# Kernel optimization log

Measured on AMD Instinct MI355X. Metric: run time of the kernel, lower is better.

The kernel has to match this reference:

```python
import jax, jax.numpy as jnp
import numpy as np

B, T, V, E, U = 64, 128, 20000, 512, 1024


def _gru_dir(x_tbe, W, Uw, bi, bh):
    """Keras GRU (reset_after=True, gate order z,r,h). x_tbe: [T,B,E]."""
    # Precompute all input projections in one big GEMM: [T,B,3U]
    xg = jnp.einsum('tbe,eg->tbg', x_tbe, W) + bi

    def step(h, xg_t):
        hg = h @ Uw + bh                       # [B,3U]
        xz, xr, xh = jnp.split(xg_t, 3, axis=-1)
        hz, hr, hh = jnp.split(hg, 3, axis=-1)
        z = jax.nn.sigmoid(xz + hz)            # update gate
        r = jax.nn.sigmoid(xr + hr)            # reset gate
        hcand = jnp.tanh(xh + r * hh)          # reset_after=True form
        h_new = z * h + (1.0 - z) * hcand
        return h_new, h_new

    h0 = jnp.zeros((x_tbe.shape[1], Uw.shape[0]), x_tbe.dtype)
    hT, outs = jax.lax.scan(step, h0, xg)      # outs: [T,B,U]
    return outs, hT


def setup_inputs() -> dict:
    key = jax.random.key(0)
    ks = jax.random.split(key, 8)
    s_in = 1.0 / np.sqrt(E)
    s_rec = 1.0 / np.sqrt(U)
    return {
        'tokens': jax.random.randint(ks[0], (B, T), 0, V),
        'emb': jax.random.normal(ks[1], (V, E), jnp.float32) * 0.05,
        'Wf': jax.random.normal(ks[2], (E, 3 * U), jnp.float32) * s_in,
        'Uf': jax.random.normal(ks[3], (U, 3 * U), jnp.float32) * s_rec,
        'bif': jnp.zeros((3 * U,), jnp.float32),
        'bhf': jnp.zeros((3 * U,), jnp.float32),
        'Wb': jax.random.normal(ks[4], (E, 3 * U), jnp.float32) * s_in,
        'Ub': jax.random.normal(ks[5], (U, 3 * U), jnp.float32) * s_rec,
        'bib': jnp.zeros((3 * U,), jnp.float32),
        'bhb': jnp.zeros((3 * U,), jnp.float32),
    }


def reference(tokens, emb, Wf, Uf, bif, bhf, Wb, Ub, bib, bhb):
    tokens = tokens[:, ::-1]                    # tf.reverse(inputs, [-1])
    x = emb[tokens]                             # embedding lookup -> [B,T,E]
    x_t = jnp.swapaxes(x, 0, 1)                 # [T,B,E]
    out_f, h_f = _gru_dir(x_t, Wf, Uf, bif, bhf)
    out_b, h_b = _gru_dir(x_t[::-1], Wb, Ub, bib, bhb)
    out_b = out_b[::-1]                         # re-align backward outputs
    outputs = jnp.swapaxes(out_f + out_b, 0, 1)  # merge_mode='sum' -> [B,T,U]
    hidden = jnp.concatenate([h_f, h_b], axis=1)  # [B,2U]
    return outputs, hidden
```

## Files before the change

kernel.cpp:

```cpp
#include <hip/hip_runtime.h>
#include <hip/hip_bf16.h>

typedef float f32;
typedef __hip_bfloat16 bf16;
typedef unsigned int u32;
typedef unsigned short u16;

#define T_LEN 128
#define B_SZ  64
#define E_DIM 512
#define U_DIM 1024
#define G3    3072
#define BTU   (B_SZ * T_LEN * U_DIM)

typedef __attribute__((ext_vector_type(8))) __bf16 bf16x8;
typedef __attribute__((ext_vector_type(8))) u16  us8;
typedef __attribute__((ext_vector_type(4))) u16  us4;
typedef __attribute__((ext_vector_type(4))) f32  f32x4;

union F8 { us8 u; bf16x8 b; };

#define WS_USW 0u
#define WS_HQ  25165824u
#define WS_XG  26214400u

#define STEP_LDS 98304
#define XG_LDS   66048

__device__ __forceinline__ u32 f32_to_bf16_rne(f32 x) {
  u32 b = __float_as_uint(x);
  return (b + 0x7fffu + ((b >> 16) & 1u)) >> 16;
}

__global__ __launch_bounds__(256) void transpose_split(
    const f32* __restrict__ Uf, const f32* __restrict__ Ub, u16* __restrict__ USW)
{
  __shared__ f32 tile[32][33];
  const int d = blockIdx.z;
  const f32* Uw = d ? Ub : Uf;
  const int c0 = blockIdx.x * 32;
  const int k0 = blockIdx.y * 32;
  const int tx = threadIdx.x & 31;
  const int ty = threadIdx.x >> 5;
#pragma unroll
  for (int i = 0; i < 4; i++) {
    int kl = ty + i * 8;
    tile[kl][tx] = Uw[(size_t)(k0 + kl) * G3 + c0 + tx];
  }
  __syncthreads();
#pragma unroll
  for (int i = 0; i < 4; i++) {
    int cl = ty + i * 8;
    int c  = c0 + cl;
    f32 val = tile[tx][cl];
    int g = c >> 10, u = c & 1023;
    int blk = d * 128 + (u >> 3);
    int r   = g * 8 + (u & 7);
    u32 hib = f32_to_bf16_rne(val);
    f32 rem = val - __uint_as_float(hib << 16);
    u32 lob = f32_to_bf16_rne(rem);
    int k = k0 + tx;
    int slot = (k >> 3) ^ (r & 7);
    size_t base = ((size_t)blk * 2) * (24 * 1024);
    size_t off  = (size_t)r * 1024 + slot * 8 + (k & 7);
    USW[base + off] = (u16)hib;
    USW[base + (size_t)24 * 1024 + off] = (u16)lob;
  }
}

__global__ __launch_bounds__(256) void xg_gemm_mfma(
    const int* __restrict__ tokens, const f32* __restrict__ emb,
    const f32* __restrict__ Wf, const f32* __restrict__ bif,
    const f32* __restrict__ Wb, const f32* __restrict__ bib,
    bf16* __restrict__ XG)
{
  extern __shared__ u16 XL[];
  u16* Ash = XL;
  u16* Bsh = XL + 16384;
  int* tok_s = (int*)(XL + 32768);

  const int tid = threadIdx.x;
  const int n0 = blockIdx.x * 128;
  const int by = blockIdx.y;
  const int dir = by >> 6;
  const int s0 = (by & 63) * 2;
  const f32* W  = dir ? Wb : Wf;
  const f32* bi = dir ? bib : bif;

  if (tid < 128) {
    int srow = s0 + (tid >> 6);
    int b = tid & 63;
    int t_orig = dir ? srow : (T_LEN - 1 - srow);
    tok_s[tid] = tokens[b * T_LEN + t_orig];
  }
  __syncthreads();

  const int wv = tid >> 6;
  const int lane = tid & 63;
  const int arow = tid >> 1;
  const int akoff = (tid & 1) * 32;
  const int bcol = tid & 127;
  const int bkoff = (tid >> 7) * 32;

  f32x4 acc[2][8];
#pragma unroll
  for (int mi = 0; mi < 2; mi++)
#pragma unroll
    for (int ni = 0; ni < 8; ni++) acc[mi][ni] = (f32x4){0.f, 0.f, 0.f, 0.f};

  const f32* asrc0 = emb + (size_t)tok_s[arow] * E_DIM + akoff;

  for (int kk = 0; kk < 8; kk++) {
    __syncthreads();
    {
      const f32* src = asrc0 + kk * 64;
#pragma unroll
      for (int g = 0; g < 4; g++) {
        float4 v0 = *(const float4*)(src + g * 8);
        float4 v1 = *(const float4*)(src + g * 8 + 4);
        f32 vv[8] = {v0.x,v0.y,v0.z,v0.w,v1.x,v1.y,v1.z,v1.w};
        us8 h8, l8;
#pragma unroll
        for (int e = 0; e < 8; e++) {
          u32 bb = __float_as_uint(vv[e]);
          h8[e] = (u16)(bb >> 16);
          f32 rem = vv[e] - __uint_as_float(bb & 0xffff0000u);
          l8[e] = (u16)f32_to_bf16_rne(rem);
        }
        int sl = (((akoff >> 3) + g) ^ (arow & 7)) * 8;
        *(us8*)&Ash[(size_t)arow * 64 + sl] = h8;
        *(us8*)&Ash[(size_t)(128 + arow) * 64 + sl] = l8;
      }
    }
    {
      const f32* src = W + (size_t)(kk * 64 + bkoff) * G3 + n0 + bcol;
#pragma unroll
      for (int g = 0; g < 4; g++) {
        us8 h8, l8;
#pragma unroll
        for (int e = 0; e < 8; e++) {
          f32 v = src[(size_t)(g * 8 + e) * G3];
          u32 bb = __float_as_uint(v);
          h8[e] = (u16)(bb >> 16);
          f32 rem = v - __uint_as_float(bb & 0xffff0000u);
          l8[e] = (u16)f32_to_bf16_rne(rem);
        }
        int sl = (((bkoff >> 3) + g) ^ (bcol & 7)) * 8;
        *(us8*)&Bsh[(size_t)bcol * 64 + sl] = h8;
        *(us8*)&Bsh[(size_t)(128 + bcol) * 64 + sl] = l8;
      }
    }
    __syncthreads();
#pragma unroll
    for (int ks = 0; ks < 2; ks++) {
      F8 ah[2], al[2];
#pragma unroll
      for (int mi = 0; mi < 2; mi++) {
        int row = wv * 32 + mi * 16 + (lane & 15);
        int sl = ((ks * 4 + (lane >> 4)) ^ (row & 7)) * 8;
        ah[mi].u = *(const us8*)&Ash[(size_t)row * 64 + sl];
        al[mi].u = *(const us8*)&Ash[(size_t)(128 + row) * 64 + sl];
      }
#pragma unroll
      for (int ni = 0; ni < 8; ni++) {
        int col = ni * 16 + (lane & 15);
        int sl = ((ks * 4 + (lane >> 4)) ^ (col & 7)) * 8;
        F8 bh, bl;
        bh.u = *(const us8*)&Bsh[(size_t)col * 64 + sl];
        bl.u = *(const us8*)&Bsh[(size_t)(128 + col) * 64 + sl];
#pragma unroll
        for (int mi = 0; mi < 2; mi++) {
          acc[mi][ni] = __builtin_amdgcn_mfma_f32_16x16x32_bf16(ah[mi].b, bh.b, acc[mi][ni], 0, 0, 0);
          acc[mi][ni] = __builtin_amdgcn_mfma_f32_16x16x32_bf16(ah[mi].b, bl.b, acc[mi][ni], 0, 0, 0);
          acc[mi][ni] = __builtin_amdgcn_mfma_f32_16x16x32_bf16(al[mi].b, bh.b, acc[mi][ni], 0, 0, 0);
        }
      }
    }
  }
#pragma unroll
  for (int ni = 0; ni < 8; ni++) {
    int ncol = n0 + ni * 16 + (lane & 15);
    f32 bv = bi[ncol];
#pragma unroll
    for (int mi = 0; mi < 2; mi++) {
#pragma unroll
      for (int j = 0; j < 4; j++) {
        int row = wv * 32 + mi * 16 + (lane >> 4) * 4 + j;
        int srow = s0 + (row >> 6);
        int b = row & 63;
        XG[((size_t)(dir * T_LEN + srow) * B_SZ + b) * G3 + ncol] =
            __float2bfloat16(acc[mi][ni][j] + bv);
      }
    }
  }
}

__global__ __launch_bounds__(512) void gru_step5(
    const u16* __restrict__ USW,
    u32* __restrict__ Hq,
    const u16* __restrict__ XG,
    const f32* __restrict__ bhf, const f32* __restrict__ bhb,
    f32* __restrict__ out, int s)
{
  extern __shared__ u16 Us[];
  const int blk = blockIdx.x;
  const int dir = blk >> 7;
  const int su  = (blk & 127) * 8;
  const int tid = threadIdx.x;
  const int lane = tid & 63;
  const int w  = tid >> 6;
  const int nw = w & 3, kw = w >> 2;

  {
    const us8* src = (const us8*)(USW + (size_t)blk * (2 * 24 * 1024));
    us8* dst = (us8*)Us;
    for (int i = tid; i < 6144; i += 512) dst[i] = src[i];
  }

  const u32* Hin  = Hq + (size_t)((s & 1) * 2 + dir) * (U_DIM * B_SZ);
  u32*       Hout = Hq + (size_t)(((s + 1) & 1) * 2 + dir) * (U_DIM * B_SZ);

  const int bb = nw * 16 + (lane & 15);
  const int ko = (lane >> 4) * 8;
  const int r0 = lane & 15;
  const int r1t = 16 + (lane & 15);
  const int r1 = r1t > 23 ? 23 : r1t;

  const int rb_h0 = (0 * 24 + r0) * 2048;
  const int rb_l0 = (1 * 24 + r0) * 2048;
  const int rb_h1 = (0 * 24 + r1) * 2048;
  const int rb_l1 = (1 * 24 + r1) * 2048;
  const int sw0 = r0 & 7, sw1 = r1 & 7;

  __syncthreads();

  f32x4 acc0 = {0.f, 0.f, 0.f, 0.f};
  f32x4 acc1 = {0.f, 0.f, 0.f, 0.f};

  if (s) {
    for (int ks = 0; ks < 16; ks++) {
      const int kb = kw * 512 + ks * 32;
      const int slot = (kb >> 3) + (lane >> 4);
      F8 ah0, al0, ah1, al1;
      ah0.u = *(const us8*)((const char*)Us + rb_h0 + ((slot ^ sw0) << 4));
      al0.u = *(const us8*)((const char*)Us + rb_l0 + ((slot ^ sw0) << 4));
      ah1.u = *(const us8*)((const char*)Us + rb_h1 + ((slot ^ sw1) << 4));
      al1.u = *(const us8*)((const char*)Us + rb_l1 + ((slot ^ sw1) << 4));

      const int kbase = kb + ko;
      u32 wd[8];
#pragma unroll
      for (int e = 0; e < 8; e++) wd[e] = Hin[(size_t)(kbase + e) * B_SZ + bb];
      F8 bh_hi, bh_lo;
#pragma unroll
      for (int e = 0; e < 8; e++) {
        bh_hi.u[e] = (u16)(wd[e] & 0xffffu);
        bh_lo.u[e] = (u16)(wd[e] >> 16);
      }
      acc0 = __builtin_amdgcn_mfma_f32_16x16x32_bf16(ah0.b, bh_hi.b, acc0, 0, 0, 0);
      acc0 = __builtin_amdgcn_mfma_f32_16x16x32_bf16(ah0.b, bh_lo.b, acc0, 0, 0, 0);
      acc0 = __builtin_amdgcn_mfma_f32_16x16x32_bf16(al0.b, bh_hi.b, acc0, 0, 0, 0);
      acc1 = __builtin_amdgcn_mfma_f32_16x16x32_bf16(ah1.b, bh_hi.b, acc1, 0, 0, 0);
      acc1 = __builtin_amdgcn_mfma_f32_16x16x32_bf16(ah1.b, bh_lo.b, acc1, 0, 0, 0);
      acc1 = __builtin_amdgcn_mfma_f32_16x16x32_bf16(al1.b, bh_hi.b, acc1, 0, 0, 0);
    }
  }

  __syncthreads();
  f32* red = (f32*)Us;
  if (kw == 1) {
    f32* p = red + (size_t)(nw * 64 + lane) * 8;
    *(f32x4*)p = acc0;
    *(f32x4*)(p + 4) = acc1;
  }
  __syncthreads();
  if (kw == 0) {
    const f32* p = red + (size_t)(nw * 64 + lane) * 8;
    f32x4 o0 = *(const f32x4*)p;
    f32x4 o1 = *(const f32x4*)(p + 4);
#pragma unroll
    for (int i = 0; i < 4; i++) { acc0[i] += o0[i]; acc1[i] += o1[i]; }

    f32 racc[4];
#pragma unroll
    for (int j = 0; j < 4; j++) racc[j] = __shfl_xor(acc0[j], 32);

    if (lane < 32) {
      const int ul0 = (lane >> 4) * 4;
      const int u0 = su + ul0;
      const u16* xgp = XG + ((size_t)(dir * T_LEN + s) * B_SZ + bb) * G3;
      us4 gz = *(const us4*)(xgp + u0);
      us4 gr = *(const us4*)(xgp + 1024 + u0);
      us4 gh = *(const us4*)(xgp + 2048 + u0);
      const f32* bh = dir ? bhb : bhf;
      f32x4 hnv;
#pragma unroll
      for (int j = 0; j < 4; j++) {
        const int u = u0 + j;
        f32 hz = acc0[j] + bh[u];
        f32 hr = racc[j] + bh[1024 + u];
        f32 hh = acc1[j] + bh[2048 + u];
        f32 xz = __uint_as_float((u32)gz[j] << 16);
        f32 xr = __uint_as_float((u32)gr[j] << 16);
        f32 xh = __uint_as_float((u32)gh[j] << 16);

        u32 hw = s ? Hin[(size_t)u * B_SZ + bb] : 0u;
        f32 hold = __uint_as_float(hw << 16) + __uint_as_float(hw & 0xffff0000u);

        f32 z  = 1.f / (1.f + expf(-(xz + hz)));
        f32 r  = 1.f / (1.f + expf(-(xr + hr)));
        f32 hc = tanhf(xh + r * hh);
        f32 hnew = z * hold + (1.f - z) * hc;

        u32 hib = f32_to_bf16_rne(hnew);
        f32 rem = hnew - __uint_as_float(hib << 16);
        u32 lob = f32_to_bf16_rne(rem);
        Hout[(size_t)u * B_SZ + bb] = hib | (lob << 16);
        hnv[j] = hnew;
      }

      const int t = dir ? (T_LEN - 1 - s) : s;
      f32* op = out + ((size_t)bb * T_LEN + t) * U_DIM + u0;
      if (s < 64) {
        *(f32x4*)op = hnv;
      } else {
        f32x4 prev = *(const f32x4*)op;
#pragma unroll
        for (int j = 0; j < 4; j++) prev[j] += hnv[j];
        *(f32x4*)op = prev;
      }
      if (s == T_LEN - 1)
        *(f32x4*)(out + (size_t)BTU + (size_t)bb * 2048 + dir * 1024 + u0) = hnv;
    }
  }
}

extern "C" void kernel_launch(void* const* d_in, const int* in_sizes, int n_in,
                              void* d_out, int out_size, void* d_ws, size_t ws_size,
                              hipStream_t stream) {
  (void)in_sizes; (void)n_in; (void)out_size; (void)ws_size;
  const int* tokens = (const int*)d_in[0];
  const f32* emb = (const f32*)d_in[1];
  const f32* Wf  = (const f32*)d_in[2];
  const f32* Uf  = (const f32*)d_in[3];
  const f32* bif = (const f32*)d_in[4];
  const f32* bhf = (const f32*)d_in[5];
  const f32* Wb  = (const f32*)d_in[6];
  const f32* Ub  = (const f32*)d_in[7];
  const f32* bib = (const f32*)d_in[8];
  const f32* bhb = (const f32*)d_in[9];

  char* ws = (char*)d_ws;
  u16*  USW = (u16*)(ws + WS_USW);
  u32*  Hq  = (u32*)(ws + WS_HQ);
  bf16* XG  = (bf16*)(ws + WS_XG);
  f32*  out = (f32*)d_out;

  transpose_split<<<dim3(96, 32, 2), 256, 0, stream>>>(Uf, Ub, USW);

  hipFuncSetAttribute((const void*)xg_gemm_mfma,
                      hipFuncAttributeMaxDynamicSharedMemorySize, XG_LDS);
  xg_gemm_mfma<<<dim3(24, 128), 256, XG_LDS, stream>>>(tokens, emb, Wf, bif, Wb, bib, XG);

  hipFuncSetAttribute((const void*)gru_step5,
                      hipFuncAttributeMaxDynamicSharedMemorySize, STEP_LDS);
  for (int s = 0; s < T_LEN; s++)
    gru_step5<<<256, 512, STEP_LDS, stream>>>(USW, Hq, (const u16*)XG, bhf, bhb, out, s);
}
```

Measured before the change: 1.892 ms.

## Pre-split W and embeddings into bf16 hi/lo; store hidden state batch-major split planes

Adds pre-pass kernels that split W (transposed) and gathered embeddings into bf16 hi/lo planes, staged in the output buffer as scratch. The input-projection GEMM then loads them with vectorized 16-byte reads instead of converting per tile and doing strided column loads of W. The recurrent step kernel now keeps the hidden state as separate hi/lo u16 planes laid out batch-major, so the B operand is two vector loads instead of eight scalar strided u32 loads. This adds extra kernel launches and scratch traffic in exchange for cheaper inner-loop loads.

```diff
diff --git a/kernel.cpp b/kernel.cpp
--- a/kernel.cpp
+++ b/kernel.cpp
@@ -24,8 +24,9 @@
 #define WS_HQ  25165824u
 #define WS_XG  26214400u
 
+
 #define STEP_LDS 98304
-#define XG_LDS   66048
+#define XG_LDS   65536
 
 __device__ __forceinline__ u32 f32_to_bf16_rne(f32 x) {
   u32 b = __float_as_uint(x);
@@ -68,32 +69,74 @@
   }
 }
 
-__global__ __launch_bounds__(256) void xg_gemm_mfma(
-    const int* __restrict__ tokens, const f32* __restrict__ emb,
-    const f32* __restrict__ Wf, const f32* __restrict__ bif,
-    const f32* __restrict__ Wb, const f32* __restrict__ bib,
+__global__ __launch_bounds__(256) void split_w(
+    const f32* __restrict__ Wf, const f32* __restrict__ Wb, u16* __restrict__ WT)
+{
+  __shared__ f32 tile[32][33];
+  const int d = blockIdx.z;
+  const f32* W = d ? Wb : Wf;
+  const int c0 = blockIdx.x * 32;
+  const int k0 = blockIdx.y * 32;
+  const int tx = threadIdx.x & 31;
+  const int ty = threadIdx.x >> 5;
+#pragma unroll
+  for (int i = 0; i < 4; i++) {
+    int kl = ty + i * 8;
+    tile[kl][tx] = W[(size_t)(k0 + kl) * G3 + c0 + tx];
+  }
+  __syncthreads();
+#pragma unroll
+  for (int i = 0; i < 4; i++) {
+    int cl = ty + i * 8;
+    f32 val = tile[tx][cl];
+    u32 bb = __float_as_uint(val);
+    u16 hi = (u16)(bb >> 16);
+    f32 rem = val - __uint_as_float(bb & 0xffff0000u);
+    u16 lo = (u16)f32_to_bf16_rne(rem);
+    size_t ch = (((size_t)(d * 2 + 0) * G3) + c0 + cl) * 512 + k0 + tx;
+    size_t cl_ = (((size_t)(d * 2 + 1) * G3) + c0 + cl) * 512 + k0 + tx;
+    WT[ch] = hi;
+    WT[cl_] = lo;
+  }
+}
+
+__global__ __launch_bounds__(128) void split_emb(
+    const int* __restrict__ tokens, const f32* __restrict__ emb, u16* __restrict__ XE)
+{
+  const int row = blockIdx.x;
+  const int b = row >> 7, t = row & 127;
+  const int tok = tokens[(size_t)b * T_LEN + t];
+  const int k = threadIdx.x * 4;
+  float4 v = *(const float4*)(emb + (size_t)tok * E_DIM + k);
+  f32 vv[4] = {v.x, v.y, v.z, v.w};
+  us4 h4, l4;
+#pragma unroll
+  for (int e = 0; e < 4; e++) {
+    u32 bb = __float_as_uint(vv[e]);
+    h4[e] = (u16)(bb >> 16);
+    f32 rem = vv[e] - __uint_as_float(bb & 0xffff0000u);
+    l4[e] = (u16)f32_to_bf16_rne(rem);
+  }
+  *(us4*)(XE + ((size_t)(0 * 64 + b) * 128 + t) * 512 + k) = h4;
+  *(us4*)(XE + ((size_t)(1 * 64 + b) * 128 + t) * 512 + k) = l4;
+}
+
+__global__ __launch_bounds__(256) void xg_gemm_mfma2(
+    const u16* __restrict__ XE,
+    const u16* __restrict__ WT,
+    const f32* __restrict__ bif, const f32* __restrict__ bib,
     bf16* __restrict__ XG)
 {
   extern __shared__ u16 XL[];
   u16* Ash = XL;
   u16* Bsh = XL + 16384;
-  int* tok_s = (int*)(XL + 32768);
 
   const int tid = threadIdx.x;
   const int n0 = blockIdx.x * 128;
   const int by = blockIdx.y;
   const int dir = by >> 6;
   const int s0 = (by & 63) * 2;
-  const f32* W  = dir ? Wb : Wf;
   const f32* bi = dir ? bib : bif;
-
-  if (tid < 128) {
-    int srow = s0 + (tid >> 6);
-    int b = tid & 63;
-    int t_orig = dir ? srow : (T_LEN - 1 - srow);
-    tok_s[tid] = tokens[b * T_LEN + t_orig];
-  }
-  __syncthreads();
 
   const int wv = tid >> 6;
   const int lane = tid & 63;
@@ -102,53 +145,37 @@
   const int bcol = tid & 127;
   const int bkoff = (tid >> 7) * 32;
 
+  const int srow = s0 + (arow >> 6);
+  const int ab = arow & 63;
+  const int at = dir ? srow : (T_LEN - 1 - srow);
+  const u16* asrc_h = XE + ((size_t)(0 * 64 + ab) * 128 + at) * 512 + akoff;
+  const u16* asrc_l = XE + ((size_t)(1 * 64 + ab) * 128 + at) * 512 + akoff;
+  const u16* bsrc_h = WT + ((size_t)(dir * 2 + 0) * G3 + n0 + bcol) * 512 + bkoff;
+  const u16* bsrc_l = WT + ((size_t)(dir * 2 + 1) * G3 + n0 + bcol) * 512 + bkoff;
+
   f32x4 acc[2][8];
 #pragma unroll
   for (int mi = 0; mi < 2; mi++)
 #pragma unroll
     for (int ni = 0; ni < 8; ni++) acc[mi][ni] = (f32x4){0.f, 0.f, 0.f, 0.f};
-
-  const f32* asrc0 = emb + (size_t)tok_s[arow] * E_DIM + akoff;
 
   for (int kk = 0; kk < 8; kk++) {
     __syncthreads();
-    {
-      const f32* src = asrc0 + kk * 64;
-#pragma unroll
-      for (int g = 0; g < 4; g++) {
-        float4 v0 = *(const float4*)(src + g * 8);
-        float4 v1 = *(const float4*)(src + g * 8 + 4);
-        f32 vv[8] = {v0.x,v0.y,v0.z,v0.w,v1.x,v1.y,v1.z,v1.w};
-        us8 h8, l8;
-#pragma unroll
-        for (int e = 0; e < 8; e++) {
-          u32 bb = __float_as_uint(vv[e]);
-          h8[e] = (u16)(bb >> 16);
-          f32 rem = vv[e] - __uint_as_float(bb & 0xffff0000u);
-          l8[e] = (u16)f32_to_bf16_rne(rem);
-        }
-        int sl = (((akoff >> 3) + g) ^ (arow & 7)) * 8;
-        *(us8*)&Ash[(size_t)arow * 64 + sl] = h8;
-        *(us8*)&Ash[(size_t)(128 + arow) * 64 + sl] = l8;
-      }
-    }
-    {
-      const f32* src = W + (size_t)(kk * 64 + bkoff) * G3 + n0 + bcol;
-#pragma unroll
-      for (int g = 0; g < 4; g++) {
-        us8 h8, l8;
-#pragma unroll
-        for (int e = 0; e < 8; e++) {
-          f32 v = src[(size_t)(g * 8 + e) * G3];
-          u32 bb = __float_as_uint(v);
-          h8[e] = (u16)(bb >> 16);
-          f32 rem = v - __uint_as_float(bb & 0xffff0000u);
-          l8[e] = (u16)f32_to_bf16_rne(rem);
-        }
-        int sl = (((bkoff >> 3) + g) ^ (bcol & 7)) * 8;
-        *(us8*)&Bsh[(size_t)bcol * 64 + sl] = h8;
-        *(us8*)&Bsh[(size_t)(128 + bcol) * 64 + sl] = l8;
-      }
+#pragma unroll
+    for (int g = 0; g < 4; g++) {
+      us8 h8 = *(const us8*)(asrc_h + kk * 64 + g * 8);
+      us8 l8 = *(const us8*)(asrc_l + kk * 64 + g * 8);
+      int sl = (((akoff >> 3) + g) ^ (arow & 7)) * 8;
+      *(us8*)&Ash[(size_t)arow * 64 + sl] = h8;
+      *(us8*)&Ash[(size_t)(128 + arow) * 64 + sl] = l8;
+    }
+#pragma unroll
+    for (int g = 0; g < 4; g++) {
+      us8 h8 = *(const us8*)(bsrc_h + kk * 64 + g * 8);
+      us8 l8 = *(const us8*)(bsrc_l + kk * 64 + g * 8);
+      int sl = (((bkoff >> 3) + g) ^ (bcol & 7)) * 8;
+      *(us8*)&Bsh[(size_t)bcol * 64 + sl] = h8;
+      *(us8*)&Bsh[(size_t)(128 + bcol) * 64 + sl] = l8;
     }
     __syncthreads();
 #pragma unroll
@@ -186,18 +213,18 @@
 #pragma unroll
       for (int j = 0; j < 4; j++) {
         int row = wv * 32 + mi * 16 + (lane >> 4) * 4 + j;
-        int srow = s0 + (row >> 6);
+        int sr = s0 + (row >> 6);
         int b = row & 63;
-        XG[((size_t)(dir * T_LEN + srow) * B_SZ + b) * G3 + ncol] =
+        XG[((size_t)(dir * T_LEN + sr) * B_SZ + b) * G3 + ncol] =
             __float2bfloat16(acc[mi][ni][j] + bv);
       }
     }
   }
 }
 
-__global__ __launch_bounds__(512) void gru_step5(
+__global__ __launch_bounds__(512) void gru_step6(
     const u16* __restrict__ USW,
-    u32* __restrict__ Hq,
+    u16* __restrict__ Hq2,
     const u16* __restrict__ XG,
     const f32* __restrict__ bhf, const f32* __restrict__ bhb,
     f32* __restrict__ out, int s)
@@ -217,11 +244,9 @@
     for (int i = tid; i < 6144; i += 512) dst[i] = src[i];
   }
 
-  const u32* Hin  = Hq + (size_t)((s & 1) * 2 + dir) * (U_DIM * B_SZ);
-  u32*       Hout = Hq + (size_t)(((s + 1) & 1) * 2 + dir) * (U_DIM * B_SZ);
-
   const int bb = nw * 16 + (lane & 15);
   const int ko = (lane >> 4) * 8;
+  const int kq = kw * 512;
   const int r0 = lane & 15;
   const int r1t = 16 + (lane & 15);
   const int r1 = r1t > 23 ? 23 : r1t;
@@ -232,6 +257,10 @@
   const int rb_l1 = (1 * 24 + r1) * 2048;
   const int sw0 = r0 & 7, sw1 = r1 & 7;
 
+  const int bufr = s & 1, bufw = bufr ^ 1;
+  const u16* HrHi = Hq2 + (size_t)(((bufr * 2 + 0) * 2 + dir) * 64 + bb) * 1024;
+  const u16* HrLo = Hq2 + (size_t)(((bufr * 2 + 1) * 2 + dir) * 64 + bb) * 1024;
+
   __syncthreads();
 
   f32x4 acc0 = {0.f, 0.f, 0.f, 0.f};
@@ -239,7 +268,7 @@
 
   if (s) {
     for (int ks = 0; ks < 16; ks++) {
-      const int kb = kw * 512 + ks * 32;
+      const int kb = kq + ks * 32;
       const int slot = (kb >> 3) + (lane >> 4);
       F8 ah0, al0, ah1, al1;
       ah0.u = *(const us8*)((const char*)Us + rb_h0 + ((slot ^ sw0) << 4));
@@ -247,16 +276,10 @@
       ah1.u = *(const us8*)((const char*)Us + rb_h1 + ((slot ^ sw1) << 4));
       al1.u = *(const us8*)((const char*)Us + rb_l1 + ((slot ^ sw1) << 4));
 
-      const int kbase = kb + ko;
-      u32 wd[8];
-#pragma unroll
-      for (int e = 0; e < 8; e++) wd[e] = Hin[(size_t)(kbase + e) * B_SZ + bb];
       F8 bh_hi, bh_lo;
-#pragma unroll
-      for (int e = 0; e < 8; e++) {
-        bh_hi.u[e] = (u16)(wd[e] & 0xffffu);
-        bh_lo.u[e] = (u16)(wd[e] >> 16);
-      }
+      bh_hi.u = *(const us8*)(HrHi + kb + ko);
+      bh_lo.u = *(const us8*)(HrLo + kb + ko);
+
       acc0 = __builtin_amdgcn_mfma_f32_16x16x32_bf16(ah0.b, bh_hi.b, acc0, 0, 0, 0);
       acc0 = __builtin_amdgcn_mfma_f32_16x16x32_bf16(ah0.b, bh_lo.b, acc0, 0, 0, 0);
       acc0 = __builtin_amdgcn_mfma_f32_16x16x32_bf16(al0.b, bh_hi.b, acc0, 0, 0, 0);
@@ -292,8 +315,14 @@
       us4 gz = *(const us4*)(xgp + u0);
       us4 gr = *(const us4*)(xgp + 1024 + u0);
       us4 gh = *(const us4*)(xgp + 2048 + u0);
+      us4 ohi = {0, 0, 0, 0}, olo = {0, 0, 0, 0};
+      if (s) {
+        ohi = *(const us4*)(HrHi + u0);
+        olo = *(const us4*)(HrLo + u0);
+      }
       const f32* bh = dir ? bhb : bhf;
       f32x4 hnv;
+      us4 whi, wlo;
 #pragma unroll
       for (int j = 0; j < 4; j++) {
         const int u = u0 + j;
@@ -303,9 +332,7 @@
         f32 xz = __uint_as_float((u32)gz[j] << 16);
         f32 xr = __uint_as_float((u32)gr[j] << 16);
         f32 xh = __uint_as_float((u32)gh[j] << 16);
-
-        u32 hw = s ? Hin[(size_t)u * B_SZ + bb] : 0u;
-        f32 hold = __uint_as_float(hw << 16) + __uint_as_float(hw & 0xffff0000u);
+        f32 hold = __uint_as_float((u32)ohi[j] << 16) + __uint_as_float((u32)olo[j] << 16);
 
         f32 z  = 1.f / (1.f + expf(-(xz + hz)));
         f32 r  = 1.f / (1.f + expf(-(xr + hr)));
@@ -315,9 +342,14 @@
         u32 hib = f32_to_bf16_rne(hnew);
         f32 rem = hnew - __uint_as_float(hib << 16);
         u32 lob = f32_to_bf16_rne(rem);
-        Hout[(size_t)u * B_SZ + bb] = hib | (lob << 16);
         hnv[j] = hnew;
-      }
+        whi[j] = (u16)hib;
+        wlo[j] = (u16)lob;
+      }
+      u16* HwHi = Hq2 + (size_t)(((bufw * 2 + 0) * 2 + dir) * 64 + bb) * 1024;
+      u16* HwLo = Hq2 + (size_t)(((bufw * 2 + 1) * 2 + dir) * 64 + bb) * 1024;
+      *(us4*)(HwHi + u0) = whi;
+      *(us4*)(HwLo + u0) = wlo;
 
       const int t = dir ? (T_LEN - 1 - s) : s;
       f32* op = out + ((size_t)bb * T_LEN + t) * U_DIM + u0;
@@ -352,18 +384,23 @@
 
   char* ws = (char*)d_ws;
   u16*  USW = (u16*)(ws + WS_USW);
-  u32*  Hq  = (u32*)(ws + WS_HQ);
+  u16*  Hq2 = (u16*)(ws + WS_HQ);
   bf16* XG  = (bf16*)(ws + WS_XG);
   f32*  out = (f32*)d_out;
 
+  u16* WT = (u16*)d_out;
+  u16* XE = (u16*)((char*)d_out + 12582912);
+
+  split_w<<<dim3(96, 16, 2), 256, 0, stream>>>(Wf, Wb, WT);
+  split_emb<<<8192, 128, 0, stream>>>(tokens, emb, XE);
   transpose_split<<<dim3(96, 32, 2), 256, 0, stream>>>(Uf, Ub, USW);
 
-  hipFuncSetAttribute((const void*)xg_gemm_mfma,
+  hipFuncSetAttribute((const void*)xg_gemm_mfma2,
                       hipFuncAttributeMaxDynamicSharedMemorySize, XG_LDS);
-  xg_gemm_mfma<<<dim3(24, 128), 256, XG_LDS, stream>>>(tokens, emb, Wf, bif, Wb, bib, XG);
-
-  hipFuncSetAttribute((const void*)gru_step5,
+  xg_gemm_mfma2<<<dim3(24, 128), 256, XG_LDS, stream>>>(XE, WT, bif, bib, XG);
+
+  hipFuncSetAttribute((const void*)gru_step6,
                       hipFuncAttributeMaxDynamicSharedMemorySize, STEP_LDS);
   for (int s = 0; s < T_LEN; s++)
-    gru_step5<<<256, 512, STEP_LDS, stream>>>(USW, Hq, (const u16*)XG, bhf, bhb, out, s);
-}
+    gru_step6<<<256, 512, STEP_LDS, stream>>>(USW, Hq2, (const u16*)XG, bhf, bhb, out, s);
+}
```

After: 2.275 ms. +20.2%, slower.
